# Performance work log

Measured on AMD Instinct MI355X. Metric: run time of the kernel, lower is better.

The kernel has to match this reference:

```python
import jax, jax.numpy as jnp
import numpy as np

D_IN, H1, H2, B, K = 128, 128, 64, 262144, 4

def _mk(key, shape):
    return jax.random.normal(key, shape, dtype=jnp.float32) * 0.05

def setup_inputs() -> dict:
    key = jax.random.key(0)
    ks = jax.random.split(key, 40)
    inp = {
        'x': jax.random.normal(ks[0], (B, 96), dtype=jnp.float32),
        'u': jax.random.normal(ks[1], (B, 32), dtype=jnp.float32),
        'mix_factor': jax.random.uniform(ks[2], (1,), dtype=jnp.float32),
        'teacher_P': jax.random.uniform(ks[3], (K,), dtype=jnp.float32),
    }
    # main critic params (torch Linear: W [out,in], b [out])
    dims = [(H1, D_IN), (H1, H1), (H2, H1), (1, H2)] * 2  # l1..l4, l5..l8
    for i, (o, ii) in enumerate(dims):
        inp[f'W{i+1}'] = _mk(ks[4 + 2 * i], (o, ii))
        inp[f'b{i+1}'] = _mk(ks[5 + 2 * i], (o,))
    # stacked teacher params (K teachers), only l1,l2,l3,l5,l6,l7 are used
    tdims = {'1': (H1, D_IN), '2': (H1, H1), '3': (H2, H1), '5': (H1, D_IN), '6': (H1, H1), '7': (H2, H1)}
    j = 20
    for name, (o, ii) in tdims.items():
        inp[f'tW{name}'] = _mk(ks[j], (K, o, ii)); j += 1
        inp[f'tb{name}'] = _mk(ks[j], (K, o)); j += 1
    return inp

def reference(x, u, mix_factor, teacher_P, W1, b1, W2, b2, W3, b3, W4, b4, W5, b5, W6, b6, W7, b7, W8, b8, tW1, tb1, tW2, tb2, tW3, tb3, tW5, tb5, tW6, tb6, tW7, tb7):
    m = mix_factor  # [1], broadcasts
    P = teacher_P   # [K]
    xu = jnp.concatenate([x, u], axis=1)  # [B, 128]

    lin = lambda h, W, b: h @ W.T + b
    # teacher linear on shared input [B,I] -> [K,B,O]
    tlin0 = lambda h, W, b: jnp.einsum('bi,koi->kbo', h, W) + b[:, None, :]
    # teacher linear on per-teacher streams [K,B,I] -> [K,B,O]
    tlin = lambda h, W, b: jnp.einsum('kbi,koi->kbo', h, W) + b[:, None, :]
    mixsum = lambda ht: jnp.einsum('kbo,k->bo', ht, P)

    def head(W_a, b_a, W_b, b_b, W_c, b_c, W_d, b_d, tWa, tba, tWb, tbb, tWc, tbc):
        ht = tlin0(xu, tWa, tba)                                   # [K,B,128]
        h = jax.nn.relu(lin(xu, W_a, b_a) * (1 - m) + mixsum(ht) * m)
        ht = jax.nn.relu(ht)
        ht2 = tlin(ht, tWb, tbb)
        h = jax.nn.relu(lin(h, W_b, b_b) * (1 - m) + mixsum(ht2) * m)
        ht2 = jax.nn.relu(ht2)
        ht3 = tlin(ht2, tWc, tbc)
        h = jax.nn.relu(lin(h, W_c, b_c) * (1 - m) + mixsum(ht3) * m)
        return lin(h, W_d, b_d)                                    # [B,1]

    x1 = head(W1, b1, W2, b2, W3, b3, W4, b4, tW1, tb1, tW2, tb2, tW3, tb3)
    x2 = head(W5, b5, W6, b6, W7, b7, W8, b8, tW5, tb5, tW6, tb6, tW7, tb7)
    return (x1, x2)
```

## Files before the change

kernel.cpp:

```cpp
#include <hip/hip_runtime.h>
#include <hip/hip_bf16.h>
#include <stdint.h>

#define B_TOTAL 262144
#define TB 64
#define RECORD 1280
#define LDS_BYTES 81920
#define HEAD_W 204800

typedef short v8s __attribute__((ext_vector_type(8)));
typedef float v4f __attribute__((ext_vector_type(4)));

union Frag { uint4 q; uint32_t d[4]; v8s v; };

__device__ __forceinline__ uint32_t pack2(float a, float b) {
    union { __hip_bfloat162 h; uint32_t u; } p;
    p.h = __float22bfloat162_rn(make_float2(a, b));
    return p.u;
}


struct KParams {
    const float* x; const float* u; const float* mix; const float* P;
    const float* mb[6];
    const float* tb[6];
    const float* Wout[2];
    const float* bout[2];
    const unsigned short* wbf;
    float* out;
};

struct PrepParams { const float* src[12]; unsigned short* dst; };

__global__ __launch_bounds__(256) void prep_kernel(PrepParams pp) {
    const int ends[12] = {16384,81920,98304,163840,172032,204800,
                          221184,286720,303104,368640,376832,409600};
    int gi = (blockIdx.x * 256 + threadIdx.x) * 4;
    if (gi >= 409600) return;
    int s = 0;
    #pragma unroll
    for (int i = 0; i < 12; ++i) { if (gi >= ends[i]) s = i + 1; }
    int base = (s == 0) ? 0 : ends[s - 1];
    const float4 f = *(const float4*)(pp.src[s] + (gi - base));
    *(uint2*)(pp.dst + gi) = make_uint2(pack2(f.x, f.y), pack2(f.z, f.w));
}

__device__ __forceinline__ void stage_xu(char* lds, const float* x, const float* u,
                                         int rowBase, int tid)
{
    for (int G = tid; G < 1024; G += 512) {
        const int row = G >> 4;
        const int gg  = G & 15;
        const int grow = rowBase + row;
        float4 fa, fb;
        if (gg < 12) {
            const float* s2 = x + grow * 96 + gg * 8;
            fa = *(const float4*)s2; fb = *(const float4*)(s2 + 4);
        } else {
            const float* s2 = u + grow * 32 + (gg - 12) * 8;
            fa = *(const float4*)s2; fb = *(const float4*)(s2 + 4);
        }
        *(uint4*)(lds + row * RECORD + ((gg ^ (row & 15)) << 4)) =
            make_uint4(pack2(fa.x, fa.y), pack2(fa.z, fa.w),
                       pack2(fb.x, fb.y), pack2(fb.z, fb.w));
    }
}

struct WPre { Frag w[20]; float4 mB; float4 tB[4]; };

template<int N>
__device__ __forceinline__ WPre preload(const unsigned short* W, int colBase,
        const float* mbias, const float* tbias, int lane)
{
    WPre r;
    const int l15  = lane & 15;
    const int quad = lane >> 4;
    const unsigned short* wRow = W + (colBase + l15) * 128 + quad * 8;
    #pragma unroll
    for (int s = 0; s < 5; ++s)
        #pragma unroll
        for (int ks = 0; ks < 4; ++ks)
            r.w[s * 4 + ks].q = *(const uint4*)(wRow + s * (N * 128) + ks * 32);
    const int obase = colBase + quad * 4;
    r.mB = *(const float4*)(mbias + obase);
    #pragma unroll
    for (int s = 0; s < 4; ++s)
        r.tB[s] = *(const float4*)(tbias + s * N + obase);
    return r;
}

template<bool SHARED_IN, int NBT>
__device__ __forceinline__ void mfma_phase(const char* lds, uint32_t btOff,
        const WPre& wp, v4f (&acc)[5][NBT], int lane)
{
    const int l15  = lane & 15;
    const int quad = lane >> 4;

    const uint32_t rb = (uint32_t)l15 * RECORD + ((uint32_t)l15 << 4) + btOff;
    uint32_t rA[4];
    #pragma unroll
    for (int ks = 0; ks < 4; ++ks)
        rA[ks] = rb ^ (uint32_t)(((ks << 2) | quad) << 4);

    #pragma unroll
    for (int bt = 0; bt < NBT; ++bt) {
        acc[0][bt] = (v4f){wp.mB.x, wp.mB.y, wp.mB.z, wp.mB.w};
        #pragma unroll
        for (int s = 0; s < 4; ++s)
            acc[s + 1][bt] = (v4f){wp.tB[s].x, wp.tB[s].y, wp.tB[s].z, wp.tB[s].w};
    }

    #pragma unroll
    for (int ks = 0; ks < 4; ++ks) {
        Frag xS[NBT];
        if constexpr (SHARED_IN) {
            #pragma unroll
            for (int bt = 0; bt < NBT; ++bt)
                xS[bt].q = *(const uint4*)(lds + rA[ks] + (uint32_t)(bt * 20480));
        }
        #pragma unroll
        for (int s = 0; s < 5; ++s) {
            Frag xF[NBT];
            if constexpr (!SHARED_IN) {
                #pragma unroll
                for (int bt = 0; bt < NBT; ++bt)
                    xF[bt].q = *(const uint4*)(lds + rA[ks]
                                + (uint32_t)(bt * 20480 + s * 256));
            }
            #pragma unroll
            for (int bt = 0; bt < NBT; ++bt)
                acc[s][bt] = __builtin_amdgcn_mfma_f32_16x16x32_bf16(
                    wp.w[s * 4 + ks].v, (SHARED_IN ? xS[bt].v : xF[bt].v),
                    acc[s][bt], 0, 0, 0);
        }
    }
}

__device__ __forceinline__ void write_streams(char* lds, v4f (&acc)[5][4],
        float c0, const float* cP, int lane, int colBase)
{
    const int l15  = lane & 15;
    const int quad = lane >> 4;
    const uint32_t rb = (uint32_t)l15 * RECORD + ((uint32_t)l15 << 4);
    const int obase = colBase + (quad << 2);
    const int ocg = (colBase >> 3) + (quad >> 1);
    const uint32_t w0 = (rb ^ ((uint32_t)ocg << 4)) + (uint32_t)((quad & 1) << 3);
    #pragma unroll
    for (int bt = 0; bt < 4; ++bt) {
        char* ab = lds + (w0 + (uint32_t)(bt * 20480));
        float vr[4];
        vr[0] = c0 * acc[0][bt][0];
        vr[1] = c0 * acc[0][bt][1];
        vr[2] = c0 * acc[0][bt][2];
        vr[3] = c0 * acc[0][bt][3];
        uint2 tw[4];
        #pragma unroll
        for (int s = 0; s < 4; ++s) {
            const float t0 = acc[s + 1][bt][0];
            const float t1 = acc[s + 1][bt][1];
            const float t2 = acc[s + 1][bt][2];
            const float t3 = acc[s + 1][bt][3];
            vr[0] = fmaf(cP[s], t0, vr[0]);
            vr[1] = fmaf(cP[s], t1, vr[1]);
            vr[2] = fmaf(cP[s], t2, vr[2]);
            vr[3] = fmaf(cP[s], t3, vr[3]);
            tw[s] = make_uint2(pack2(fmaxf(t0, 0.f), fmaxf(t1, 0.f)),
                               pack2(fmaxf(t2, 0.f), fmaxf(t3, 0.f)));
        }
        *(uint2*)ab = make_uint2(pack2(fmaxf(vr[0], 0.f), fmaxf(vr[1], 0.f)),
                                 pack2(fmaxf(vr[2], 0.f), fmaxf(vr[3], 0.f)));
        #pragma unroll
        for (int s = 0; s < 4; ++s)
            *(uint2*)(ab + (1 + s) * 256) = tw[s];
    }
}

extern "C" __global__ __launch_bounds__(512, 2)
void critic_kernel(KParams p)
{
    extern __shared__ char lds[];
    const int tid  = threadIdx.x;
    const int lane = tid & 63;
    const int wave = tid >> 6;
    const int rowBase = blockIdx.x * TB;

    const int cb128 = wave << 4;
    const int cb64  = (wave >> 1) << 4;
    const int btB64 = (wave & 1) << 1;
    const uint32_t btOff64 = (uint32_t)btB64 * 20480u;

    const float m  = p.mix[0];
    const float c0 = 1.f - m;
    float cP[4];
    #pragma unroll
    for (int k = 0; k < 4; ++k) cP[k] = m * p.P[k];

    stage_xu(lds, p.x, p.u, rowBase, tid);

    #pragma unroll 1
    for (int head = 0; head < 2; ++head) {
        const unsigned short* wb = p.wbf + head * HEAD_W;
        const int hb = head * 3;
        v4f acc[5][4];

        WPre w1 = preload<128>(wb, cb128, p.mb[hb + 0], p.tb[hb + 0], lane);
        __syncthreads();
        mfma_phase<true, 4>(lds, 0, w1, acc, lane);
        __syncthreads();
        write_streams(lds, acc, c0, cP, lane, cb128);
        WPre w2 = preload<128>(wb + 81920, cb128, p.mb[hb + 1], p.tb[hb + 1], lane);
        __syncthreads();
        mfma_phase<false, 4>(lds, 0, w2, acc, lane);
        __syncthreads();
        write_streams(lds, acc, c0, cP, lane, cb128);
        WPre w3 = preload<64>(wb + 163840, cb64, p.mb[hb + 2], p.tb[hb + 2], lane);
        __syncthreads();
        v4f accF[5][2];
        mfma_phase<false, 2>(lds, btOff64, w3, accF, lane);
        {
            const int obase = cb64 + ((lane >> 4) << 2);
            const float4 wo = *(const float4*)(p.Wout[head] + obase);
            float psum[2];
            #pragma unroll
            for (int j = 0; j < 2; ++j) {
                float vr[4];
                vr[0] = c0 * accF[0][j][0];
                vr[1] = c0 * accF[0][j][1];
                vr[2] = c0 * accF[0][j][2];
                vr[3] = c0 * accF[0][j][3];
                #pragma unroll
                for (int s = 0; s < 4; ++s) {
                    vr[0] = fmaf(cP[s], accF[s + 1][j][0], vr[0]);
                    vr[1] = fmaf(cP[s], accF[s + 1][j][1], vr[1]);
                    vr[2] = fmaf(cP[s], accF[s + 1][j][2], vr[2]);
                    vr[3] = fmaf(cP[s], accF[s + 1][j][3], vr[3]);
                }
                float pp = fmaxf(vr[0], 0.f) * wo.x + fmaxf(vr[1], 0.f) * wo.y
                         + fmaxf(vr[2], 0.f) * wo.z + fmaxf(vr[3], 0.f) * wo.w;
                pp += __shfl_xor(pp, 16);
                pp += __shfl_xor(pp, 32);
                psum[j] = pp;
            }
            __syncthreads();
            if (lane < 16) {
                float* pgrid = (float*)(lds + 256);
                #pragma unroll
                for (int j = 0; j < 2; ++j)
                    pgrid[(cb64 >> 4) * 64 + (btB64 + j) * 16 + lane] = psum[j];
            }
        }
        if (head == 0) {
            stage_xu(lds, p.x, p.u, rowBase, tid);
        }
        __syncthreads();
        if (tid < 64) {
            const float* pg = (const float*)(lds + 256);
            p.out[head * B_TOTAL + rowBase + tid] =
                p.bout[head][0] + pg[tid] + pg[64 + tid] + pg[128 + tid] + pg[192 + tid];
        }
    }
}

extern "C" void kernel_launch(void* const* d_in, const int* in_sizes, int n_in,
                              void* d_out, int out_size, void* d_ws, size_t ws_size,
                              hipStream_t stream)
{
    (void)in_sizes; (void)n_in; (void)out_size; (void)ws_size;

    PrepParams pp;
    const int sidx[12] = {4, 20, 6, 22, 8, 24, 12, 26, 14, 28, 16, 30};
    for (int i = 0; i < 12; ++i) pp.src[i] = (const float*)d_in[sidx[i]];
    pp.dst = (unsigned short*)d_ws;

    KParams kp;
    kp.x = (const float*)d_in[0];  kp.u = (const float*)d_in[1];
    kp.mix = (const float*)d_in[2]; kp.P = (const float*)d_in[3];
    const int mbi[6] = {5, 7, 9, 13, 15, 17};
    const int tbi[6] = {21, 23, 25, 27, 29, 31};
    for (int i = 0; i < 6; ++i) {
        kp.mb[i] = (const float*)d_in[mbi[i]];
        kp.tb[i] = (const float*)d_in[tbi[i]];
    }
    kp.Wout[0] = (const float*)d_in[10]; kp.Wout[1] = (const float*)d_in[18];
    kp.bout[0] = (const float*)d_in[11]; kp.bout[1] = (const float*)d_in[19];
    kp.wbf = (const unsigned short*)d_ws;
    kp.out = (float*)d_out;

    (void)hipFuncSetAttribute((const void*)critic_kernel,
                              hipFuncAttributeMaxDynamicSharedMemorySize, LDS_BYTES);

    hipLaunchKernelGGL(prep_kernel, dim3(400), dim3(256), 0, stream, pp);
    hipLaunchKernelGGL(critic_kernel, dim3(B_TOTAL / TB), dim3(512), LDS_BYTES, stream, kp);
}
```

Measured before the change: 873.8 us.

## Interleave both critic heads layer by layer with a doubled LDS record

Doubles the per-row LDS record so both heads' activation streams can live side by side. The kernel now processes head 0 and head 1 interleaved: each barrier interval writes one head's streams while running the other head's MFMA phase. The xu input is staged only once and shared by both heads, and the number of block-wide barriers drops. In exchange LDS per block doubles to 160 KB, which likely limits the kernel to one 512-thread block per CU instead of two, trading occupancy for intra-block overlap.

```diff
diff --git a/kernel.cpp b/kernel.cpp
--- a/kernel.cpp
+++ b/kernel.cpp
@@ -4,8 +4,8 @@
 
 #define B_TOTAL 262144
 #define TB 64
-#define RECORD 1280
-#define LDS_BYTES 81920
+#define RECORD 2560
+#define LDS_BYTES 163840
 #define HEAD_W 204800
 
 typedef short v8s __attribute__((ext_vector_type(8)));
@@ -89,13 +89,12 @@
     return r;
 }
 
-template<bool SHARED_IN, int NBT>
+template<bool SHARED_IN, int SM, int ST, int NBT>
 __device__ __forceinline__ void mfma_phase(const char* lds, uint32_t btOff,
         const WPre& wp, v4f (&acc)[5][NBT], int lane)
 {
     const int l15  = lane & 15;
     const int quad = lane >> 4;
-
     const uint32_t rb = (uint32_t)l15 * RECORD + ((uint32_t)l15 << 4) + btOff;
     uint32_t rA[4];
     #pragma unroll
@@ -116,16 +115,19 @@
         if constexpr (SHARED_IN) {
             #pragma unroll
             for (int bt = 0; bt < NBT; ++bt)
-                xS[bt].q = *(const uint4*)(lds + rA[ks] + (uint32_t)(bt * 20480));
+                xS[bt].q = *(const uint4*)(lds + rA[ks]
+                            + (uint32_t)(bt * 40960 + SM * 256));
         }
         #pragma unroll
         for (int s = 0; s < 5; ++s) {
+            constexpr int dummy = 0; (void)dummy;
             Frag xF[NBT];
             if constexpr (!SHARED_IN) {
+                const int slot = (s == 0) ? SM : (ST + s - 1);
                 #pragma unroll
                 for (int bt = 0; bt < NBT; ++bt)
                     xF[bt].q = *(const uint4*)(lds + rA[ks]
-                                + (uint32_t)(bt * 20480 + s * 256));
+                                + (uint32_t)(bt * 40960 + slot * 256));
             }
             #pragma unroll
             for (int bt = 0; bt < NBT; ++bt)
@@ -136,18 +138,18 @@
     }
 }
 
+template<int WM, int WT>
 __device__ __forceinline__ void write_streams(char* lds, v4f (&acc)[5][4],
         float c0, const float* cP, int lane, int colBase)
 {
     const int l15  = lane & 15;
     const int quad = lane >> 4;
     const uint32_t rb = (uint32_t)l15 * RECORD + ((uint32_t)l15 << 4);
-    const int obase = colBase + (quad << 2);
     const int ocg = (colBase >> 3) + (quad >> 1);
     const uint32_t w0 = (rb ^ ((uint32_t)ocg << 4)) + (uint32_t)((quad & 1) << 3);
     #pragma unroll
     for (int bt = 0; bt < 4; ++bt) {
-        char* ab = lds + (w0 + (uint32_t)(bt * 20480));
+        char* ab = lds + (w0 + (uint32_t)(bt * 40960));
         float vr[4];
         vr[0] = c0 * acc[0][bt][0];
         vr[1] = c0 * acc[0][bt][1];
@@ -167,11 +169,41 @@
             tw[s] = make_uint2(pack2(fmaxf(t0, 0.f), fmaxf(t1, 0.f)),
                                pack2(fmaxf(t2, 0.f), fmaxf(t3, 0.f)));
         }
-        *(uint2*)ab = make_uint2(pack2(fmaxf(vr[0], 0.f), fmaxf(vr[1], 0.f)),
-                                 pack2(fmaxf(vr[2], 0.f), fmaxf(vr[3], 0.f)));
+        *(uint2*)(ab + WM * 256) =
+            make_uint2(pack2(fmaxf(vr[0], 0.f), fmaxf(vr[1], 0.f)),
+                       pack2(fmaxf(vr[2], 0.f), fmaxf(vr[3], 0.f)));
         #pragma unroll
         for (int s = 0; s < 4; ++s)
-            *(uint2*)(ab + (1 + s) * 256) = tw[s];
+            *(uint2*)(ab + (WT + s) * 256) = tw[s];
+    }
+}
+
+__device__ __forceinline__ void psum_write(const v4f (&accF)[5][2], float c0,
+        const float* cP, const float* Wout, float* pgrid, int lane,
+        int cb64, int btB64)
+{
+    const int obase = cb64 + ((lane >> 4) << 2);
+    const float4 wo = *(const float4*)(Wout + obase);
+    #pragma unroll
+    for (int j = 0; j < 2; ++j) {
+        float vr[4];
+        vr[0] = c0 * accF[0][j][0];
+        vr[1] = c0 * accF[0][j][1];
+        vr[2] = c0 * accF[0][j][2];
+        vr[3] = c0 * accF[0][j][3];
+        #pragma unroll
+        for (int s = 0; s < 4; ++s) {
+            vr[0] = fmaf(cP[s], accF[s + 1][j][0], vr[0]);
+            vr[1] = fmaf(cP[s], accF[s + 1][j][1], vr[1]);
+            vr[2] = fmaf(cP[s], accF[s + 1][j][2], vr[2]);
+            vr[3] = fmaf(cP[s], accF[s + 1][j][3], vr[3]);
+        }
+        float pp = fmaxf(vr[0], 0.f) * wo.x + fmaxf(vr[1], 0.f) * wo.y
+                 + fmaxf(vr[2], 0.f) * wo.z + fmaxf(vr[3], 0.f) * wo.w;
+        pp += __shfl_xor(pp, 16);
+        pp += __shfl_xor(pp, 32);
+        if (lane < 16)
+            pgrid[(cb64 >> 4) * 64 + (btB64 + j) * 16 + lane] = pp;
     }
 }
 
@@ -187,7 +219,7 @@
     const int cb128 = wave << 4;
     const int cb64  = (wave >> 1) << 4;
     const int btB64 = (wave & 1) << 1;
-    const uint32_t btOff64 = (uint32_t)btB64 * 20480u;
+    const uint32_t btOff64 = (uint32_t)btB64 * 40960u;
 
     const float m  = p.mix[0];
     const float c0 = 1.f - m;
@@ -195,69 +227,69 @@
     #pragma unroll
     for (int k = 0; k < 4; ++k) cP[k] = m * p.P[k];
 
+    const unsigned short* wb0 = p.wbf;
+    const unsigned short* wb1 = p.wbf + HEAD_W;
+
     stage_xu(lds, p.x, p.u, rowBase, tid);
-
-    #pragma unroll 1
-    for (int head = 0; head < 2; ++head) {
-        const unsigned short* wb = p.wbf + head * HEAD_W;
-        const int hb = head * 3;
-        v4f acc[5][4];
-
-        WPre w1 = preload<128>(wb, cb128, p.mb[hb + 0], p.tb[hb + 0], lane);
-        __syncthreads();
-        mfma_phase<true, 4>(lds, 0, w1, acc, lane);
-        __syncthreads();
-        write_streams(lds, acc, c0, cP, lane, cb128);
-        WPre w2 = preload<128>(wb + 81920, cb128, p.mb[hb + 1], p.tb[hb + 1], lane);
-        __syncthreads();
-        mfma_phase<false, 4>(lds, 0, w2, acc, lane);
-        __syncthreads();
-        write_streams(lds, acc, c0, cP, lane, cb128);
-        WPre w3 = preload<64>(wb + 163840, cb64, p.mb[hb + 2], p.tb[hb + 2], lane);
-        __syncthreads();
-        v4f accF[5][2];
-        mfma_phase<false, 2>(lds, btOff64, w3, accF, lane);
-        {
-            const int obase = cb64 + ((lane >> 4) << 2);
-            const float4 wo = *(const float4*)(p.Wout[head] + obase);
-            float psum[2];
-            #pragma unroll
-            for (int j = 0; j < 2; ++j) {
-                float vr[4];
-                vr[0] = c0 * accF[0][j][0];
-                vr[1] = c0 * accF[0][j][1];
-                vr[2] = c0 * accF[0][j][2];
-                vr[3] = c0 * accF[0][j][3];
-                #pragma unroll
-                for (int s = 0; s < 4; ++s) {
-                    vr[0] = fmaf(cP[s], accF[s + 1][j][0], vr[0]);
-                    vr[1] = fmaf(cP[s], accF[s + 1][j][1], vr[1]);
-                    vr[2] = fmaf(cP[s], accF[s + 1][j][2], vr[2]);
-                    vr[3] = fmaf(cP[s], accF[s + 1][j][3], vr[3]);
-                }
-                float pp = fmaxf(vr[0], 0.f) * wo.x + fmaxf(vr[1], 0.f) * wo.y
-                         + fmaxf(vr[2], 0.f) * wo.z + fmaxf(vr[3], 0.f) * wo.w;
-                pp += __shfl_xor(pp, 16);
-                pp += __shfl_xor(pp, 32);
-                psum[j] = pp;
-            }
-            __syncthreads();
-            if (lane < 16) {
-                float* pgrid = (float*)(lds + 256);
-                #pragma unroll
-                for (int j = 0; j < 2; ++j)
-                    pgrid[(cb64 >> 4) * 64 + (btB64 + j) * 16 + lane] = psum[j];
-            }
-        }
-        if (head == 0) {
-            stage_xu(lds, p.x, p.u, rowBase, tid);
-        }
-        __syncthreads();
-        if (tid < 64) {
-            const float* pg = (const float*)(lds + 256);
-            p.out[head * B_TOTAL + rowBase + tid] =
-                p.bout[head][0] + pg[tid] + pg[64 + tid] + pg[128 + tid] + pg[192 + tid];
-        }
+    WPre wA = preload<128>(wb0, cb128, p.mb[0], p.tb[0], lane);
+    __syncthreads();
+
+    v4f accB[5][4];
+    {
+        WPre wB = preload<128>(wb1, cb128, p.mb[3], p.tb[3], lane);
+        v4f accA[5][4];
+        mfma_phase<true, 0, 0, 4>(lds, 0, wA, accA, lane);
+        write_streams<1, 2>(lds, accA, c0, cP, lane, cb128);
+        mfma_phase<true, 0, 0, 4>(lds, 0, wB, accB, lane);
+    }
+    __syncthreads();
+
+    v4f accC[5][4];
+    {
+        WPre wC = preload<128>(wb0 + 81920, cb128, p.mb[1], p.tb[1], lane);
+        write_streams<0, 6>(lds, accB, c0, cP, lane, cb128);
+        mfma_phase<false, 1, 2, 4>(lds, 0, wC, accC, lane);
+    }
+    __syncthreads();
+
+    v4f accD[5][4];
+    {
+        WPre wD = preload<128>(wb1 + 81920, cb128, p.mb[4], p.tb[4], lane);
+        write_streams<1, 2>(lds, accC, c0, cP, lane, cb128);
+        mfma_phase<false, 0, 6, 4>(lds, 0, wD, accD, lane);
+    }
+    __syncthreads();
+
+    v4f accE[5][2];
+    {
+        WPre wE = preload<64>(wb0 + 163840, cb64, p.mb[2], p.tb[2], lane);
+        write_streams<0, 6>(lds, accD, c0, cP, lane, cb128);
+        mfma_phase<false, 1, 2, 2>(lds, btOff64, wE, accE, lane);
+    }
+    __syncthreads();
+
+    v4f accF[5][2];
+    {
+        WPre wF = preload<64>(wb1 + 163840, cb64, p.mb[5], p.tb[5], lane);
+        psum_write(accE, c0, cP, p.Wout[0], (float*)(lds + 256),
+                   lane, cb64, btB64);
+        mfma_phase<false, 0, 6, 2>(lds, btOff64, wF, accF, lane);
+    }
+    __syncthreads();
+
+    if (tid < 64) {
+        const float* pg = (const float*)(lds + 256);
+        p.out[rowBase + tid] =
+            p.bout[0][0] + pg[tid] + pg[64 + tid] + pg[128 + tid] + pg[192 + tid];
+    }
+    psum_write(accF, c0, cP, p.Wout[1], (float*)(lds + 1536),
+               lane, cb64, btB64);
+    __syncthreads();
+
+    if (tid < 64) {
+        const float* pg = (const float*)(lds + 1536);
+        p.out[B_TOTAL + rowBase + tid] =
+            p.bout[1][0] + pg[tid] + pg[64 + tid] + pg[128 + tid] + pg[192 + tid];
     }
 }
 
```

Result: faster. 786.5 us (-10.0%).
